# Optimization experiments

Measured on AMD Instinct MI355X. Metric: run time of the kernel, lower is better.

## Reference

```python
import jax, jax.numpy as jnp
import numpy as np
import math

C_S = 384; C_Z = 128; C_H = 16; H = 12; PQ = 4; PV = 8; C_SURF = 16
N_RES = 512; N_SURF = 2048; B = 1
INF = 1e5; EPS = 1e-8
SOFTPLUS_INV_1 = 0.541324854612918


def _quat_to_rot(q):
    q = q / jnp.linalg.norm(q, axis=-1, keepdims=True)
    w, x, y, z = q[..., 0], q[..., 1], q[..., 2], q[..., 3]
    R = jnp.stack([
        1 - 2 * (y * y + z * z), 2 * (x * y - w * z), 2 * (x * z + w * y),
        2 * (x * y + w * z), 1 - 2 * (x * x + z * z), 2 * (y * z - w * x),
        2 * (x * z - w * y), 2 * (y * z + w * x), 1 - 2 * (x * x + y * y),
    ], axis=-1)
    return R.reshape(q.shape[:-1] + (3, 3))


def setup_inputs() -> dict:
    key = jax.random.key(0)
    ks = jax.random.split(key, 32)
    hc = H * C_H            # 192
    hpq = H * PQ * 3        # 144
    hpkv = H * (PQ + PV) * 3  # 432
    cz4 = C_Z // 4
    concat = hc + H * PV * 3 + H * PV + H * cz4 + hc  # 1152
    w = lambda k, i, o: jax.random.normal(k, (i, o), jnp.float32) * 0.02
    inp = {
        's': jax.random.normal(ks[0], (B, N_RES, C_S), jnp.float32),
        'z': jax.random.normal(ks[1], (B, N_RES, N_RES, C_Z), jnp.float32),
        'rots': _quat_to_rot(jax.random.normal(ks[2], (B, N_RES, 4), jnp.float32)),
        'trans': jax.random.normal(ks[3], (B, N_RES, 3), jnp.float32) * 10.0,
        'mask': jnp.ones((B, N_RES), jnp.float32),
        'surface_points': jax.random.normal(ks[4], (B, N_SURF, 3), jnp.float32) * 10.0,
        'surface_features': jax.random.normal(ks[5], (B, N_SURF, C_SURF), jnp.float32),
        'surface_mask': jnp.ones((B, N_SURF), jnp.float32),
        'Wq': w(ks[6], C_S, hc), 'bq': jnp.zeros((hc,)),
        'Wkv': w(ks[7], C_S, 2 * hc), 'bkv': jnp.zeros((2 * hc,)),
        'Wqp': w(ks[8], C_S, hpq), 'bqp': jnp.zeros((hpq,)),
        'Wkvp': w(ks[9], C_S, hpkv), 'bkvp': jnp.zeros((hpkv,)),
        'Wse': w(ks[10], C_SURF, C_S), 'bse': jnp.zeros((C_S,)),
        'Wsq': w(ks[11], C_S, hc), 'bsq': jnp.zeros((hc,)),
        'Wsk': w(ks[12], C_S, hc), 'bsk': jnp.zeros((hc,)),
        'Wsv': w(ks[13], C_S, hc), 'bsv': jnp.zeros((hc,)),
        'Wb': w(ks[14], C_Z, H), 'bb': jnp.zeros((H,)),
        'Wdz': w(ks[15], C_Z, cz4), 'bdz': jnp.zeros((cz4,)),
        'head_weights': jnp.full((H,), SOFTPLUS_INV_1, jnp.float32),
        'sb_weights': jnp.full((1,), SOFTPLUS_INV_1, jnp.float32),
        'Wout': w(ks[16], concat, C_S), 'bout': jnp.zeros((C_S,)),
        'Wso': w(ks[17], 2 * C_S, C_SURF), 'bso': jnp.zeros((C_SURF,)),
    }
    return inp


def reference(s, z, rots, trans, mask, surface_points, surface_features, surface_mask,
              Wq, bq, Wkv, bkv, Wqp, bqp, Wkvp, bkvp, Wse, bse, Wsq, bsq, Wsk, bsk,
              Wsv, bsv, Wb, bb, Wdz, bdz, head_weights, sb_weights, Wout, bout, Wso, bso):
    lin = lambda x, W, b: x @ W + b
    b_, n, _ = s.shape
    m = surface_points.shape[-2]

    surface_feat = lin(surface_features, Wse, bse)                    # [B,M,c_s]
    # backbone<->surface squared distances
    disp = trans[:, :, None, :] - surface_points[:, None, :, :]       # [B,N,M,3]
    dist_sq = jnp.sum(disp * disp, -1)                                # [B,N,M]

    q = lin(s, Wq, bq).reshape(b_, n, H, C_H)
    kv = lin(s, Wkv, bkv).reshape(b_, n, H, 2 * C_H)
    k, v = kv[..., :C_H], kv[..., C_H:]

    # query points: split into 3 coord chunks, stack, rigid-apply
    qp = lin(s, Wqp, bqp)
    qp = jnp.stack(jnp.split(qp, 3, axis=-1), axis=-1)                # [B,N,H*PQ,3]
    qp = jnp.einsum('bnij,bnpj->bnpi', rots, qp) + trans[:, :, None]
    qp = qp.reshape(b_, n, H, PQ, 3)

    kvp = lin(s, Wkvp, bkvp)
    kvp = jnp.stack(jnp.split(kvp, 3, axis=-1), axis=-1)              # [B,N,H*(PQ+PV),3]
    kvp = jnp.einsum('bnij,bnpj->bnpi', rots, kvp) + trans[:, :, None]
    kvp = kvp.reshape(b_, n, H, PQ + PV, 3)
    kp, vp = kvp[..., :PQ, :], kvp[..., PQ:, :]

    b_bias = lin(z, Wb, bb)                                           # [B,N,N,H]
    a = jnp.einsum('bihc,bjhc->bhij', q, k) * math.sqrt(1.0 / (3 * C_H))
    a = a + math.sqrt(1.0 / 3) * jnp.transpose(b_bias, (0, 3, 1, 2))

    # point-distance attention term
    pt = jnp.sum((qp[:, :, None] - kp[:, None]) ** 2, axis=-1)        # [B,N,N,H,PQ]
    hw = jax.nn.softplus(head_weights)                                # [H]
    pt = jnp.sum(pt, axis=-1) * hw * math.sqrt(1.0 / (3 * (PQ * 9.0 / 2))) * (-0.5)
    a = a + jnp.transpose(pt, (0, 3, 1, 2))                           # [B,H,N,N]

    sq_mask = INF * (mask[:, :, None] * mask[:, None, :] - 1.0)
    a = jax.nn.softmax(a + sq_mask[:, None], axis=-1)

    o = jnp.einsum('bhij,bjhc->bihc', a, v).reshape(b_, n, H * C_H)
    o_pt = jnp.einsum('bhij,bjhpd->bihpd', a, vp)                     # [B,N,H,PV,3]
    o_pt = jnp.einsum('bnji,bnhpj->bnhpi', rots, o_pt - trans[:, :, None, None])
    o_pt_norm = jnp.sqrt(jnp.sum(o_pt ** 2, -1) + EPS).reshape(b_, n, H * PV)
    o_pt_flat = o_pt.reshape(b_, n, H * PV, 3)

    pair_z = lin(z, Wdz, bdz)                                         # [B,N,N,cz/4]
    o_pair = jnp.einsum('bhij,bijc->bihc', a, pair_z).reshape(b_, n, -1)

    # surface cross-attention branch
    sq = lin(s, Wsq, bsq).reshape(b_, n, H, C_H)
    sk = lin(surface_feat, Wsk, bsk).reshape(b_, m, H, C_H)
    sv = lin(surface_feat, Wsv, bsv).reshape(b_, m, H, C_H)
    logits = jnp.einsum('bnhc,bmhc->bhnm', sq, sk) * math.sqrt(1.0 / C_H)
    sbw = jax.nn.softplus(sb_weights)[0]
    logits = logits - 0.5 * sbw * dist_sq[:, None]
    cross_mask = mask[:, :, None] * surface_mask[:, None, :]          # [B,N,M]
    logits = logits + INF * (cross_mask - 1.0)[:, None]
    a_s = jax.nn.softmax(logits, axis=-1)
    o_surf = jnp.einsum('bhnm,bmhc->bnhc', a_s, sv).reshape(b_, n, H * C_H)

    o_cat = jnp.concatenate([o, o_pt_flat[..., 0], o_pt_flat[..., 1], o_pt_flat[..., 2],
                             o_pt_norm, o_pair, o_surf], axis=-1)
    s_out = lin(o_cat, Wout, bout)                                    # [B,N,c_s]

    # surface update: attend surface points to backbone (softmax over residues)
    a_ts = jax.nn.softmax(jnp.swapaxes(logits, -1, -2), axis=-1).mean(axis=1)  # [B,M,N]
    s_agg = jnp.einsum('bmn,bnc->bmc', a_ts, s)
    surf_out = lin(jnp.concatenate([surface_feat, s_agg], axis=-1), Wso, bso)
    return s_out, surf_out
```

## Files before the change

### kernel.cpp

```cpp
#include <hip/hip_runtime.h>
#include <cstddef>


#define CS 384
#define INFV 100000.0f

__device__ __forceinline__ float softplusf(float x) { return log1pf(__expf(x)); }

__global__ __launch_bounds__(256) void k_pack(
    const float* __restrict__ Wq, const float* __restrict__ Wsq,
    const float* __restrict__ Wkv, const float* __restrict__ Wqp,
    const float* __restrict__ Wkvp, const float* __restrict__ Wsk,
    const float* __restrict__ Wsv, const float* __restrict__ Wout,
    const float* __restrict__ bq, const float* __restrict__ bsq,
    const float* __restrict__ bkv, const float* __restrict__ bqp,
    const float* __restrict__ bkvp, const float* __restrict__ bsk,
    const float* __restrict__ bsv,
    float* __restrict__ wt1, float* __restrict__ wt2, float* __restrict__ wt3,
    float* __restrict__ b1, float* __restrict__ b2)
{
    const int b = blockIdx.x, t = threadIdx.x;
    if (b >= 1092) {
        int idx = (b - 1092) * 256 + t;
        if (idx < 1344) {
            float v;
            if (idx < 192) v = bq[idx];
            else if (idx < 384) v = bsq[idx - 192];
            else if (idx < 768) v = bkv[idx - 384];
            else if (idx < 912) v = bqp[idx - 768];
            else v = bkvp[idx - 912];
            b1[idx] = v;
        } else if (idx < 1728) {
            int i2 = idx - 1344;
            b2[i2] = (i2 < 192) ? bsk[i2] : bsv[i2 - 192];
        }
        return;
    }
    const float* src; float* dst; int C, coff, tile, ldd;
    if (b < 72)       { src = Wq;   C = 192; dst = wt1; coff = 0;   ldd = 384;  tile = b; }
    else if (b < 144) { src = Wsq;  C = 192; dst = wt1; coff = 192; ldd = 384;  tile = b - 72; }
    else if (b < 288) { src = Wkv;  C = 384; dst = wt1; coff = 384; ldd = 384;  tile = b - 144; }
    else if (b < 348) { src = Wqp;  C = 144; dst = wt1; coff = 768; ldd = 384;  tile = b - 288; }
    else if (b < 516) { src = Wkvp; C = 432; dst = wt1; coff = 912; ldd = 384;  tile = b - 348; }
    else if (b < 588) { src = Wsk;  C = 192; dst = wt2; coff = 0;   ldd = 384;  tile = b - 516; }
    else if (b < 660) { src = Wsv;  C = 192; dst = wt2; coff = 192; ldd = 384;  tile = b - 588; }
    else              { src = Wout; C = 384; dst = wt3; coff = 0;   ldd = 1152; tile = b - 660; }
    const int cT = (C + 31) >> 5;
    const int tk = tile / cT, tc = tile % cT;
    __shared__ float l[32][33];
    const int tr = t >> 5, tcc = t & 31;
    #pragma unroll
    for (int rr = 0; rr < 4; ++rr) {
        int kloc = tr * 4 + rr;
        int cg = tc * 32 + tcc;
        l[kloc][tcc] = (cg < C) ? src[(size_t)(tk * 32 + kloc) * C + cg] : 0.f;
    }
    __syncthreads();
    #pragma unroll
    for (int rr = 0; rr < 4; ++rr) {
        int cloc = tr * 4 + rr;
        int cg = tc * 32 + cloc;
        if (cg < C) dst[(size_t)(coff + cg) * ldd + tk * 32 + tcc] = l[tcc][cloc];
    }
}

__global__ __launch_bounds__(256) void k_transp(
    const float* __restrict__ A, float* __restrict__ At)
{
    __shared__ float tile[32][33];
    const int r0 = blockIdx.y * 32, c0 = blockIdx.x * 32;
    const int tr = threadIdx.x >> 5, tc = threadIdx.x & 31;
    #pragma unroll
    for (int rr = 0; rr < 4; ++rr)
        tile[tr + rr * 8][tc] = A[(size_t)(r0 + tr + rr * 8) * 384 + c0 + tc];
    __syncthreads();
    #pragma unroll
    for (int rr = 0; rr < 4; ++rr)
        At[(size_t)(c0 + tr + rr * 8) * 512 + r0 + tc] = tile[tc][tr + rr * 8];
}

template<int KTOT, bool HB>
__global__ __launch_bounds__(256) void k_gemm(
    const float* __restrict__ A, const float* __restrict__ Wt,
    const float* __restrict__ bias, float* __restrict__ C, int ldc)
{
    __shared__ float As[64][68];
    __shared__ float Ws[64][68];
    const int t = threadIdx.x;
    const int c0 = blockIdx.x * 64, m0 = blockIdx.y * 64;
    const int sr = t >> 4, sk4 = (t & 15) << 2;
    const int wid = t >> 6, lane = t & 63;
    const int wr = (wid >> 1) * 32, wc = (wid & 1) * 32;
    const int lr = lane >> 3, lc = lane & 7;
    float acc[4][4];
    #pragma unroll
    for (int j = 0; j < 4; ++j) {
        float bv = HB ? bias[c0 + wc + lc + 8 * j] : 0.f;
        #pragma unroll
        for (int i = 0; i < 4; ++i) acc[i][j] = bv;
    }
    for (int kc = 0; kc < KTOT; kc += 64) {
        __syncthreads();
        #pragma unroll
        for (int rep = 0; rep < 4; ++rep) {
            int row = sr + rep * 16;
            *(float4*)&As[row][sk4] = *(const float4*)&A[(size_t)(m0 + row) * KTOT + kc + sk4];
            *(float4*)&Ws[row][sk4] = *(const float4*)&Wt[(size_t)(c0 + row) * KTOT + kc + sk4];
        }
        __syncthreads();
        #pragma unroll 4
        for (int k4 = 0; k4 < 16; ++k4) {
            float4 a[4], w[4];
            #pragma unroll
            for (int i = 0; i < 4; ++i) a[i] = *(float4*)&As[wr + lr + 8 * i][k4 * 4];
            #pragma unroll
            for (int j = 0; j < 4; ++j) w[j] = *(float4*)&Ws[wc + lc + 8 * j][k4 * 4];
            #pragma unroll
            for (int i = 0; i < 4; ++i) {
                #pragma unroll
                for (int j = 0; j < 4; ++j) {
                    acc[i][j] = fmaf(a[i].x, w[j].x, acc[i][j]);
                    acc[i][j] = fmaf(a[i].y, w[j].y, acc[i][j]);
                    acc[i][j] = fmaf(a[i].z, w[j].z, acc[i][j]);
                    acc[i][j] = fmaf(a[i].w, w[j].w, acc[i][j]);
                }
            }
        }
    }
    #pragma unroll
    for (int i = 0; i < 4; ++i) {
        #pragma unroll
        for (int j = 0; j < 4; ++j)
            C[(size_t)(m0 + wr + lr + 8 * i) * ldc + c0 + wc + lc + 8 * j] = acc[i][j];
    }
}

__global__ __launch_bounds__(256) void k_scatter(
    const float* __restrict__ proj, const float* __restrict__ rots,
    const float* __restrict__ trans,
    float* __restrict__ qw, float* __restrict__ kw, float* __restrict__ vw,
    float* __restrict__ sqw, float* __restrict__ qpw, float* __restrict__ kpw,
    float* __restrict__ vpw)
{
    __shared__ float p[4][1344];
    const int n0 = blockIdx.x * 4, t = threadIdx.x;
    for (int idx = t; idx < 1344; idx += 256) {
        #pragma unroll
        for (int r = 0; r < 4; ++r) p[r][idx] = proj[(size_t)(n0 + r) * 1344 + idx];
    }
    __syncthreads();
    for (int idx = t; idx < 3072; idx += 256) {
        int r = idx / 768, c = idx % 768;
        int n = n0 + r;
        float v = p[r][c];
        if (c < 192) qw[(size_t)n * 192 + c] = v;
        else if (c < 384) sqw[(size_t)n * 192 + (c - 192)] = v;
        else {
            int cc = c - 384, h = cc >> 5, sub = cc & 31;
            if (sub < 16) kw[(size_t)n * 192 + h * 16 + sub] = v;
            else          vw[(size_t)n * 192 + h * 16 + (sub - 16)] = v;
        }
    }
    for (int idx = t; idx < 2304; idx += 256) {
        int r = idx / 576, rem = idx % 576;
        int n = n0 + r;
        const float* R = &rots[(size_t)n * 9];
        const float* tr = &trans[(size_t)n * 3];
        if (rem < 144) {
            int pp = rem / 3, d = rem % 3;
            float v = fmaf(R[d*3+0], p[r][768 + pp],
                      fmaf(R[d*3+1], p[r][768 + 48 + pp],
                      fmaf(R[d*3+2], p[r][768 + 96 + pp], tr[d])));
            qpw[(size_t)n * 144 + pp * 3 + d] = v;
        } else {
            int rem2 = rem - 144; int pp = rem2 / 3, d = rem2 % 3;
            float v = fmaf(R[d*3+0], p[r][912 + pp],
                      fmaf(R[d*3+1], p[r][912 + 144 + pp],
                      fmaf(R[d*3+2], p[r][912 + 288 + pp], tr[d])));
            int h = pp / 12, ii = pp % 12;
            if (ii < 4) kpw[(size_t)n * 144 + h * 12 + ii * 3 + d] = v;
            else        vpw[(size_t)n * 288 + h * 24 + (ii - 4) * 3 + d] = v;
        }
    }
}

__global__ __launch_bounds__(256) void k_sfeat(
    const float* __restrict__ sf, const float* __restrict__ Wse,
    const float* __restrict__ bse, float* __restrict__ sfeat)
{
    __shared__ float wl[16 * 384];
    __shared__ float sfl[8][16];
    const int m0 = blockIdx.x * 8, t = threadIdx.x;
    for (int idx = t; idx < 6144; idx += 256) wl[idx] = Wse[idx];
    if (t < 128) sfl[t >> 4][t & 15] = sf[(size_t)(m0 + (t >> 4)) * 16 + (t & 15)];
    __syncthreads();
    #pragma unroll
    for (int u = 0; u < 12; ++u) {
        int idx = t + u * 256;
        int r = idx / 384, c = idx % 384;
        float a = bse[c];
        #pragma unroll
        for (int kk = 0; kk < 16; ++kk) a = fmaf(sfl[r][kk], wl[kk * 384 + c], a);
        sfeat[(size_t)(m0 + r) * 384 + c] = a;
    }
}

__global__ __launch_bounds__(256) void k_zpass(
    const float* __restrict__ z, const float* __restrict__ Wb, const float* __restrict__ bb,
    const float* __restrict__ Wdz, const float* __restrict__ bdz, float* __restrict__ bpz)
{
    __shared__ float Wt[44][128];
    __shared__ float bias_s[44];
    __shared__ float zt[64][132];
    const int i = blockIdx.x, t = threadIdx.x;
    const float s3 = 0.5773502691896258f;
    for (int idx = t; idx < 44 * 128; idx += 256) {
        int c = idx >> 7, kk = idx & 127;
        Wt[c][kk] = (c < 12) ? s3 * Wb[kk * 12 + c] : Wdz[kk * 32 + (c - 12)];
    }
    if (t < 44) bias_s[t] = (t < 12) ? s3 * bb[t] : bdz[t - 12];
    const int jl = t & 63, cg = t >> 6;
    for (int j0 = 0; j0 < 512; j0 += 64) {
        __syncthreads();
        for (int idx = t; idx < 2048; idx += 256) {
            int r = idx >> 5, c4 = (idx & 31) << 2;
            *(float4*)&zt[r][c4] = *(const float4*)&z[((size_t)i * 512 + j0 + r) * 128 + c4];
        }
        __syncthreads();
        float acc[11];
        #pragma unroll
        for (int u = 0; u < 11; ++u) acc[u] = bias_s[cg * 11 + u];
        #pragma unroll 2
        for (int k4 = 0; k4 < 128; k4 += 4) {
            float4 zv = *(float4*)&zt[jl][k4];
            #pragma unroll
            for (int u = 0; u < 11; ++u) {
                float4 wv = *(float4*)&Wt[cg * 11 + u][k4];
                acc[u] = fmaf(zv.x, wv.x, acc[u]);
                acc[u] = fmaf(zv.y, wv.y, acc[u]);
                acc[u] = fmaf(zv.z, wv.z, acc[u]);
                acc[u] = fmaf(zv.w, wv.w, acc[u]);
            }
        }
        #pragma unroll
        for (int u = 0; u < 11; ++u)
            bpz[((size_t)i * 44 + cg * 11 + u) * 512 + j0 + jl] = acc[u];
    }
}

__global__ __launch_bounds__(256) void k_attn(
    const float* __restrict__ qw, const float* __restrict__ kw, const float* __restrict__ vw,
    const float* __restrict__ qpw, const float* __restrict__ kpw, const float* __restrict__ vpw,
    const float* __restrict__ bpz, const float* __restrict__ mask,
    const float* __restrict__ rots, const float* __restrict__ trans,
    const float* __restrict__ hwp, float* __restrict__ ocat)
{
    __shared__ float pls[12 * 516];
    __shared__ float qs[192], qps[144], opt[288], cpt[12], red[4];
    const int i = blockIdx.x, t = threadIdx.x;
    if (t < 192) qs[t] = qw[(size_t)i * 192 + t];
    if (t < 144) qps[t] = qpw[(size_t)i * 144 + t];
    if (t < 12) cpt[t] = -0.5f * 0.13608276348795434f * softplusf(hwp[t]);
    const float mask_i = mask[i];
    __syncthreads();
    for (int hj = t; hj < 6144; hj += 256) {
        int h = hj >> 9, j = hj & 511;
        float kj[16], kpj[12];
        { const float4* kr = (const float4*)&kw[(size_t)j * 192 + h * 16];
          *(float4*)&kj[0] = kr[0]; *(float4*)&kj[4] = kr[1];
          *(float4*)&kj[8] = kr[2]; *(float4*)&kj[12] = kr[3]; }
        { const float4* kr = (const float4*)&kpw[(size_t)j * 144 + h * 12];
          *(float4*)&kpj[0] = kr[0]; *(float4*)&kpj[4] = kr[1]; *(float4*)&kpj[8] = kr[2]; }
        float qk = 0.f;
        #pragma unroll
        for (int c = 0; c < 16; ++c) qk = fmaf(qs[h * 16 + c], kj[c], qk);
        float pts = 0.f;
        #pragma unroll
        for (int p = 0; p < 4; ++p) {
            float dx = qps[h*12+p*3+0] - kpj[p*3+0];
            float dy = qps[h*12+p*3+1] - kpj[p*3+1];
            float dz = qps[h*12+p*3+2] - kpj[p*3+2];
            pts += dx*dx + dy*dy + dz*dz;
        }
        float lg = fmaf(0.14433756729740643f, qk, bpz[((size_t)i * 44 + h) * 512 + j]);
        lg = fmaf(cpt[h], pts, lg);
        lg += INFV * (mask_i * mask[j] - 1.0f);
        pls[h * 516 + j] = lg;
    }
    __syncthreads();
    for (int h = 0; h < 12; ++h) {
        float v0 = pls[h * 516 + t], v1 = pls[h * 516 + 256 + t];
        float mx = fmaxf(v0, v1);
        #pragma unroll
        for (int off = 32; off; off >>= 1) mx = fmaxf(mx, __shfl_xor(mx, off));
        if ((t & 63) == 0) red[t >> 6] = mx;
        __syncthreads();
        mx = fmaxf(fmaxf(red[0], red[1]), fmaxf(red[2], red[3]));
        __syncthreads();
        float e0 = __expf(v0 - mx), e1 = __expf(v1 - mx);
        float sm = e0 + e1;
        #pragma unroll
        for (int off = 32; off; off >>= 1) sm += __shfl_xor(sm, off);
        if ((t & 63) == 0) red[t >> 6] = sm;
        __syncthreads();
        float inv = 1.0f / (red[0] + red[1] + red[2] + red[3]);
        pls[h * 516 + t] = e0 * inv;
        pls[h * 516 + 256 + t] = e1 * inv;
        __syncthreads();
    }
    for (int rnd = 0; rnd < 2; ++rnd) {
        int oi = t + rnd * 256;
        if (oi < 480) {
            int h, stride; const float* src;
            if (oi < 192) { h = oi >> 4; src = vw + oi; stride = 192; }
            else { h = (oi - 192) / 24; src = vpw + (oi - 192); stride = 288; }
            const float* pr = &pls[h * 516];
            float a0 = 0, a1 = 0, a2 = 0, a3 = 0;
            for (int j = 0; j < 512; j += 4) {
                a0 = fmaf(pr[j+0], src[(size_t)(j+0) * stride], a0);
                a1 = fmaf(pr[j+1], src[(size_t)(j+1) * stride], a1);
                a2 = fmaf(pr[j+2], src[(size_t)(j+2) * stride], a2);
                a3 = fmaf(pr[j+3], src[(size_t)(j+3) * stride], a3);
            }
            float acc = (a0 + a1) + (a2 + a3);
            if (oi < 192) ocat[(size_t)i * 1152 + oi] = acc;
            else opt[oi - 192] = acc;
        }
    }
    {
        int w = t >> 6, lane = t & 63;
        for (int u = 0; u < 96; ++u) {
            int oi = w * 96 + u; int h = oi >> 5, c = oi & 31;
            const float* pz = &bpz[((size_t)i * 44 + 12 + c) * 512];
            const float* pr = &pls[h * 516];
            float sacc = 0.f;
            #pragma unroll
            for (int jj = 0; jj < 8; ++jj)
                sacc = fmaf(pr[lane + jj * 64], pz[lane + jj * 64], sacc);
            #pragma unroll
            for (int off = 32; off; off >>= 1) sacc += __shfl_xor(sacc, off);
            if (lane == 0) ocat[(size_t)i * 1152 + 576 + oi] = sacc;
        }
    }
    __syncthreads();
    if (t < 96) {
        int h = t >> 3, p = t & 7;
        const float* R = &rots[(size_t)i * 9];
        float gx = opt[h*24 + p*3 + 0] - trans[(size_t)i*3 + 0];
        float gy = opt[h*24 + p*3 + 1] - trans[(size_t)i*3 + 1];
        float gz = opt[h*24 + p*3 + 2] - trans[(size_t)i*3 + 2];
        float lx = R[0]*gx + R[3]*gy + R[6]*gz;
        float ly = R[1]*gx + R[4]*gy + R[7]*gz;
        float lz = R[2]*gx + R[5]*gy + R[8]*gz;
        float nm = sqrtf(lx*lx + ly*ly + lz*lz + 1e-8f);
        int col = h * 8 + p;
        size_t base = (size_t)i * 1152;
        ocat[base + 192 + col] = lx;
        ocat[base + 288 + col] = ly;
        ocat[base + 384 + col] = lz;
        ocat[base + 480 + col] = nm;
    }
}

__global__ __launch_bounds__(256) void k_surf(
    const float* __restrict__ sqw, const float* __restrict__ skv,
    const float* __restrict__ trans, const float* __restrict__ mask,
    const float* __restrict__ sp, const float* __restrict__ smask,
    const float* __restrict__ sbwp, float* __restrict__ ocat)
{
    __shared__ float sk_t[256][17];
    __shared__ float sv_t[256][17];
    __shared__ float sp_t[768];
    __shared__ float smask_t[256];
    const int h = blockIdx.x >> 5;
    const int n0 = (blockIdx.x & 31) * 16;
    const int t = threadIdx.x;
    const int tn = t >> 4, tm = t & 15;
    const int n = n0 + tn;
    const float sbw = softplusf(sbwp[0]);
    float qreg[16];
    #pragma unroll
    for (int c = 0; c < 16; ++c) qreg[c] = sqw[(size_t)n * 192 + h * 16 + c];
    const float trx = trans[(size_t)n*3+0], tryy = trans[(size_t)n*3+1], trz = trans[(size_t)n*3+2];
    const float mask_n = mask[n];
    float mx = -1e30f, l = 0.f;
    float acc[16];
    #pragma unroll
    for (int c = 0; c < 16; ++c) acc[c] = 0.f;
    for (int tile = 0; tile < 8; ++tile) {
        __syncthreads();
        const int mb = tile * 256;
        for (int idx = t; idx < 1024; idx += 256) {
            int ml = idx >> 2, c4 = (idx & 3) << 2;
            float4 v4 = *(const float4*)&skv[(size_t)(mb + ml) * 384 + h * 16 + c4];
            sk_t[ml][c4+0]=v4.x; sk_t[ml][c4+1]=v4.y; sk_t[ml][c4+2]=v4.z; sk_t[ml][c4+3]=v4.w;
            float4 w4 = *(const float4*)&skv[(size_t)(mb + ml) * 384 + 192 + h * 16 + c4];
            sv_t[ml][c4+0]=w4.x; sv_t[ml][c4+1]=w4.y; sv_t[ml][c4+2]=w4.z; sv_t[ml][c4+3]=w4.w;
        }
        for (int idx = t; idx < 768; idx += 256) sp_t[idx] = sp[(size_t)mb * 3 + idx];
        smask_t[t] = smask[mb + t];
        __syncthreads();
        float lgr[16];
        float tmax = -1e30f;
        #pragma unroll
        for (int kk = 0; kk < 16; ++kk) {
            int ml = tm + (kk << 4);
            float dot = 0.f;
            #pragma unroll
            for (int c = 0; c < 16; ++c) dot = fmaf(qreg[c], sk_t[ml][c], dot);
            float dx = trx - sp_t[ml*3+0], dy = tryy - sp_t[ml*3+1], dz = trz - sp_t[ml*3+2];
            float lg = fmaf(0.25f, dot, -0.5f * sbw * (dx*dx + dy*dy + dz*dz));
            lg += INFV * (mask_n * smask_t[ml] - 1.0f);
            lgr[kk] = lg;
            tmax = fmaxf(tmax, lg);
        }
        float mn = fmaxf(mx, tmax);
        float scale = __expf(mx - mn);
        l *= scale;
        #pragma unroll
        for (int c = 0; c < 16; ++c) acc[c] *= scale;
        #pragma unroll
        for (int kk = 0; kk < 16; ++kk) {
            int ml = tm + (kk << 4);
            float w = __expf(lgr[kk] - mn);
            l += w;
            #pragma unroll
            for (int c = 0; c < 16; ++c) acc[c] = fmaf(w, sv_t[ml][c], acc[c]);
        }
        mx = mn;
    }
    #pragma unroll
    for (int off = 1; off < 16; off <<= 1) {
        float m2 = __shfl_xor(mx, off), l2 = __shfl_xor(l, off);
        float mn = fmaxf(mx, m2);
        float e1 = __expf(mx - mn), e2 = __expf(m2 - mn);
        l = l * e1 + l2 * e2;
        #pragma unroll
        for (int c = 0; c < 16; ++c) {
            float a2 = __shfl_xor(acc[c], off);
            acc[c] = acc[c] * e1 + a2 * e2;
        }
        mx = mn;
    }
    const float invl = 1.0f / l;
    float outv = 0.f;
    #pragma unroll
    for (int c = 0; c < 16; ++c) if (tm == c) outv = acc[c];
    ocat[(size_t)n * 1152 + 960 + h * 16 + tm] = outv * invl;
}

__global__ __launch_bounds__(256) void k_tlog(
    const float* __restrict__ sqw, const float* __restrict__ skv,
    const float* __restrict__ trans, const float* __restrict__ mask,
    const float* __restrict__ sp, const float* __restrict__ smask,
    const float* __restrict__ sbwp, float* __restrict__ logits,
    float* __restrict__ stat_m, float* __restrict__ stat_il)
{
    __shared__ float sk_s[32][16];
    __shared__ float sq_s[32][16];
    __shared__ float trans_s[96];
    __shared__ float mask_s[32];
    __shared__ float spm_s[96];
    __shared__ float smask_s[32];
    const int h = blockIdx.y;
    const int m0 = blockIdx.x * 32;
    const int t = threadIdx.x;
    const int tmg = t >> 5, tnl = t & 31;
    const float sbw = softplusf(sbwp[0]);
    for (int idx = t; idx < 512; idx += 256) {
        int row = idx >> 4, c = idx & 15;
        sk_s[row][c] = skv[(size_t)(m0 + row) * 384 + h * 16 + c];
    }
    if (t < 96) spm_s[t] = sp[(size_t)m0 * 3 + t];
    if (t < 32) smask_s[t] = smask[m0 + t];
    __syncthreads();
    float skr[4][16];
    float spx[4], spy[4], spz[4], smk[4];
    #pragma unroll
    for (int mi = 0; mi < 4; ++mi) {
        int row = tmg * 4 + mi;
        #pragma unroll
        for (int c4 = 0; c4 < 16; c4 += 4)
            *(float4*)&skr[mi][c4] = *(float4*)&sk_s[row][c4];
        spx[mi] = spm_s[row*3+0]; spy[mi] = spm_s[row*3+1]; spz[mi] = spm_s[row*3+2];
        smk[mi] = smask_s[row];
    }
    float mxr[4], lr[4];
    #pragma unroll
    for (int mi = 0; mi < 4; ++mi) { mxr[mi] = -1e30f; lr[mi] = 0.f; }
    for (int nt = 0; nt < 16; ++nt) {
        __syncthreads();
        const int nb = nt * 32;
        if (t < 128) {
            int nn = t >> 2, c4 = (t & 3) << 2;
            *(float4*)&sq_s[nn][c4] = *(const float4*)&sqw[(size_t)(nb + nn) * 192 + h * 16 + c4];
        }
        if (t < 96) trans_s[t] = trans[(size_t)nb * 3 + t];
        if (t < 32) mask_s[t] = mask[nb + t];
        __syncthreads();
        float q[16];
        #pragma unroll
        for (int c4 = 0; c4 < 16; c4 += 4)
            *(float4*)&q[c4] = *(float4*)&sq_s[tnl][c4];
        const float tx = trans_s[tnl*3+0], ty = trans_s[tnl*3+1], tz = trans_s[tnl*3+2];
        const float mkn = mask_s[tnl];
        #pragma unroll
        for (int mi = 0; mi < 4; ++mi) {
            float dot = 0.f;
            #pragma unroll
            for (int c = 0; c < 16; ++c) dot = fmaf(skr[mi][c], q[c], dot);
            float dx = tx - spx[mi], dy = ty - spy[mi], dz = tz - spz[mi];
            float mterm = INFV * (mkn * smk[mi] - 1.0f) - 0.5f * sbw * (dx*dx + dy*dy + dz*dz);
            float lg = fmaf(0.25f, dot, mterm);
            logits[((size_t)(m0 + tmg * 4 + mi) * 12 + h) * 512 + nb + tnl] = lg;
            float newm = fmaxf(mxr[mi], lg);
            lr[mi] = lr[mi] * __expf(mxr[mi] - newm) + __expf(lg - newm);
            mxr[mi] = newm;
        }
    }
    #pragma unroll
    for (int off = 1; off < 32; off <<= 1) {
        #pragma unroll
        for (int mi = 0; mi < 4; ++mi) {
            float m2 = __shfl_xor(mxr[mi], off), l2 = __shfl_xor(lr[mi], off);
            float newm = fmaxf(mxr[mi], m2);
            lr[mi] = lr[mi] * __expf(mxr[mi] - newm) + l2 * __expf(m2 - newm);
            mxr[mi] = newm;
        }
    }
    if (tnl == 0) {
        #pragma unroll
        for (int mi = 0; mi < 4; ++mi) {
            int m = m0 + tmg * 4 + mi;
            stat_m[(size_t)m * 12 + h] = mxr[mi];
            stat_il[(size_t)m * 12 + h] = 1.0f / lr[mi];
        }
    }
}

__global__ __launch_bounds__(256) void k_tw(
    const float* __restrict__ logits, const float* __restrict__ stat_m,
    const float* __restrict__ stat_il, float* __restrict__ w)
{
    __shared__ float mxs[12], ils[12];
    const int m = blockIdx.x, t = threadIdx.x;
    if (t < 12) { mxs[t] = stat_m[(size_t)m * 12 + t]; ils[t] = stat_il[(size_t)m * 12 + t]; }
    __syncthreads();
    const float* lp = logits + (size_t)m * 12 * 512;
    float a0 = 0.f, a1 = 0.f;
    #pragma unroll
    for (int h = 0; h < 12; ++h) {
        a0 += __expf(lp[h * 512 + t] - mxs[h]) * ils[h];
        a1 += __expf(lp[h * 512 + 256 + t] - mxs[h]) * ils[h];
    }
    w[(size_t)m * 512 + t] = a0 * (1.0f / 12.0f);
    w[(size_t)m * 512 + 256 + t] = a1 * (1.0f / 12.0f);
}

__global__ __launch_bounds__(256) void k_surf_out(
    const float* __restrict__ sfeat, const float* __restrict__ saggw,
    const float* __restrict__ Wso, const float* __restrict__ bso,
    float* __restrict__ out)
{
    __shared__ float wl[12304];
    const int t = threadIdx.x;
    for (int idx = t; idx < 12288; idx += 256) {
        int k = idx >> 4, c = idx & 15;
        wl[(k / 192) * 3076 + (k % 192) * 16 + c] = Wso[idx];
    }
    const int m = blockIdx.x * 64 + (t >> 2);
    const int kq = t & 3;
    const float* src = (kq < 2) ? &sfeat[(size_t)m * 384 + kq * 192]
                                : &saggw[(size_t)m * 384 + (kq - 2) * 192];
    __syncthreads();
    float acc[16];
    #pragma unroll
    for (int c = 0; c < 16; ++c) acc[c] = 0.f;
    const float* wb = &wl[kq * 3076];
    for (int k = 0; k < 192; k += 4) {
        float4 v = *(const float4*)&src[k];
        #pragma unroll
        for (int e = 0; e < 4; ++e) {
            float sv = (&v.x)[e];
            #pragma unroll
            for (int c = 0; c < 16; ++c)
                acc[c] = fmaf(sv, wb[(k + e) * 16 + c], acc[c]);
        }
    }
    #pragma unroll
    for (int c = 0; c < 16; ++c) {
        acc[c] += __shfl_xor(acc[c], 1);
        acc[c] += __shfl_xor(acc[c], 2);
    }
    #pragma unroll
    for (int c = 0; c < 16; ++c) {
        if ((c >> 2) == kq) out[196608 + (size_t)m * 16 + c] = acc[c] + bso[c];
    }
}

extern "C" void kernel_launch(void* const* d_in, const int* in_sizes, int n_in,
                              void* d_out, int out_size, void* d_ws, size_t ws_size,
                              hipStream_t stream)
{
    (void)in_sizes; (void)n_in; (void)out_size; (void)ws_size;
    const float* s     = (const float*)d_in[0];
    const float* z     = (const float*)d_in[1];
    const float* rots  = (const float*)d_in[2];
    const float* trans = (const float*)d_in[3];
    const float* mask  = (const float*)d_in[4];
    const float* sp    = (const float*)d_in[5];
    const float* sf    = (const float*)d_in[6];
    const float* smask = (const float*)d_in[7];
    const float* Wq    = (const float*)d_in[8];  const float* bq   = (const float*)d_in[9];
    const float* Wkv   = (const float*)d_in[10]; const float* bkv  = (const float*)d_in[11];
    const float* Wqp   = (const float*)d_in[12]; const float* bqp  = (const float*)d_in[13];
    const float* Wkvp  = (const float*)d_in[14]; const float* bkvp = (const float*)d_in[15];
    const float* Wse   = (const float*)d_in[16]; const float* bse  = (const float*)d_in[17];
    const float* Wsq   = (const float*)d_in[18]; const float* bsq  = (const float*)d_in[19];
    const float* Wsk   = (const float*)d_in[20]; const float* bsk  = (const float*)d_in[21];
    const float* Wsv   = (const float*)d_in[22]; const float* bsv  = (const float*)d_in[23];
    const float* Wb    = (const float*)d_in[24]; const float* bb   = (const float*)d_in[25];
    const float* Wdz   = (const float*)d_in[26]; const float* bdz  = (const float*)d_in[27];
    const float* hw    = (const float*)d_in[28]; const float* sbw  = (const float*)d_in[29];
    const float* Wout  = (const float*)d_in[30]; const float* bout = (const float*)d_in[31];
    const float* Wso   = (const float*)d_in[32]; const float* bso  = (const float*)d_in[33];
    float* out = (float*)d_out;

    float* qw    = (float*)d_ws;
    float* kw    = qw    + (size_t)512 * 192;
    float* vw    = kw    + (size_t)512 * 192;
    float* sqw   = vw    + (size_t)512 * 192;
    float* qpw   = sqw   + (size_t)512 * 192;
    float* kpw   = qpw   + (size_t)512 * 144;
    float* vpw   = kpw   + (size_t)512 * 144;
    float* sfeat = vpw   + (size_t)512 * 288;
    float* skv   = sfeat + (size_t)2048 * 384;
    float* ocat  = skv   + (size_t)2048 * 384;
    float* sagg  = ocat  + (size_t)512 * 1152;
    float* region = sagg + (size_t)2048 * 384;
    float* proj   = region;
    float* bpz    = region;
    float* logits = region;
    float* wt1   = region + (size_t)2048 * 12 * 512;
    float* wt2   = wt1   + (size_t)1344 * 384;
    float* wt3   = wt2   + (size_t)384 * 384;
    float* b1    = wt3   + (size_t)384 * 1152;
    float* b2    = b1    + 1344;
    float* st    = b2    + 384;
    float* wbuf  = st    + (size_t)384 * 512;
    float* statm = wbuf  + (size_t)2048 * 512;
    float* stati = statm + (size_t)2048 * 12;

    k_pack<<<dim3(1099), dim3(256), 0, stream>>>(Wq, Wsq, Wkv, Wqp, Wkvp, Wsk, Wsv, Wout,
        bq, bsq, bkv, bqp, bkvp, bsk, bsv, wt1, wt2, wt3, b1, b2);
    k_transp<<<dim3(12, 16), dim3(256), 0, stream>>>(s, st);
    k_gemm<384, true><<<dim3(21, 8), dim3(256), 0, stream>>>(s, wt1, b1, proj, 1344);
    k_scatter<<<dim3(128), dim3(256), 0, stream>>>(proj, rots, trans,
        qw, kw, vw, sqw, qpw, kpw, vpw);
    k_sfeat<<<dim3(256), dim3(256), 0, stream>>>(sf, Wse, bse, sfeat);
    k_gemm<384, true><<<dim3(6, 32), dim3(256), 0, stream>>>(sfeat, wt2, b2, skv, 384);
    k_zpass<<<dim3(512), dim3(256), 0, stream>>>(z, Wb, bb, Wdz, bdz, bpz);
    k_attn<<<dim3(512), dim3(256), 0, stream>>>(qw, kw, vw, qpw, kpw, vpw, bpz, mask,
        rots, trans, hw, ocat);
    k_surf<<<dim3(384), dim3(256), 0, stream>>>(sqw, skv, trans, mask, sp, smask,
        sbw, ocat);
    k_tlog<<<dim3(64, 12), dim3(256), 0, stream>>>(sqw, skv, trans, mask, sp, smask,
        sbw, logits, statm, stati);
    k_tw<<<dim3(2048), dim3(256), 0, stream>>>(logits, statm, stati, wbuf);
    k_gemm<512, false><<<dim3(6, 32), dim3(256), 0, stream>>>(wbuf, st, nullptr, sagg, 384);
    k_surf_out<<<dim3(32), dim3(256), 0, stream>>>(sfeat, sagg, Wso, bso, out);
    k_gemm<1152, true><<<dim3(6, 8), dim3(256), 0, stream>>>(ocat, wt3, bout, out, 384);
}
```

Baseline: 524.3 us.

## Split IPA attention into logits/softmax, pair, value-GEMM and finalize kernels

The monolithic per-residue attention kernel is split into four stages. Logits and softmax run per (residue, head-group) and write probabilities to a global buffer. A separate pair-aggregation kernel reads those probabilities, and a tiled GEMM computes the scalar and point value outputs with V rows reused across 64 query rows. A small finalize kernel scatters the results and applies the inverse frame transform. The aim is to replace the uncoalesced strided V reads and serial per-head softmax barriers with better parallelism and reuse. The cost is a 12x512x512 probability buffer written and re-read twice, plus extra launches.

```diff
diff --git a/kernel.cpp b/kernel.cpp
--- a/kernel.cpp
+++ b/kernel.cpp
@@ -248,23 +248,26 @@
     }
 }
 
-__global__ __launch_bounds__(256) void k_attn(
-    const float* __restrict__ qw, const float* __restrict__ kw, const float* __restrict__ vw,
-    const float* __restrict__ qpw, const float* __restrict__ kpw, const float* __restrict__ vpw,
+__global__ __launch_bounds__(256) void k_attn_a(
+    const float* __restrict__ qw, const float* __restrict__ kw,
+    const float* __restrict__ qpw, const float* __restrict__ kpw,
     const float* __restrict__ bpz, const float* __restrict__ mask,
-    const float* __restrict__ rots, const float* __restrict__ trans,
-    const float* __restrict__ hwp, float* __restrict__ ocat)
-{
-    __shared__ float pls[12 * 516];
-    __shared__ float qs[192], qps[144], opt[288], cpt[12], red[4];
-    const int i = blockIdx.x, t = threadIdx.x;
-    if (t < 192) qs[t] = qw[(size_t)i * 192 + t];
-    if (t < 144) qps[t] = qpw[(size_t)i * 144 + t];
-    if (t < 12) cpt[t] = -0.5f * 0.13608276348795434f * softplusf(hwp[t]);
+    const float* __restrict__ hwp, float* __restrict__ abuf)
+{
+    __shared__ float pls[4][520];
+    __shared__ float qs[64], qps[48], cpt4[4];
+    const int i = blockIdx.x, hg = blockIdx.y;
+    const int t = threadIdx.x;
+    if (t < 64) qs[t] = qw[(size_t)i * 192 + hg * 64 + t];
+    if (t < 48) qps[t] = qpw[(size_t)i * 144 + hg * 48 + t];
+    if (t < 4) cpt4[t] = -0.5f * 0.13608276348795434f * softplusf(hwp[hg * 4 + t]);
     const float mask_i = mask[i];
     __syncthreads();
-    for (int hj = t; hj < 6144; hj += 256) {
-        int h = hj >> 9, j = hj & 511;
+    #pragma unroll 2
+    for (int it = 0; it < 8; ++it) {
+        int idx = t + it * 256;
+        int hh = idx >> 9, j = idx & 511;
+        int h = hg * 4 + hh;
         float kj[16], kpj[12];
         { const float4* kr = (const float4*)&kw[(size_t)j * 192 + h * 16];
           *(float4*)&kj[0] = kr[0]; *(float4*)&kj[4] = kr[1];
@@ -273,82 +276,149 @@
           *(float4*)&kpj[0] = kr[0]; *(float4*)&kpj[4] = kr[1]; *(float4*)&kpj[8] = kr[2]; }
         float qk = 0.f;
         #pragma unroll
-        for (int c = 0; c < 16; ++c) qk = fmaf(qs[h * 16 + c], kj[c], qk);
+        for (int c = 0; c < 16; ++c) qk = fmaf(qs[hh * 16 + c], kj[c], qk);
         float pts = 0.f;
         #pragma unroll
         for (int p = 0; p < 4; ++p) {
-            float dx = qps[h*12+p*3+0] - kpj[p*3+0];
-            float dy = qps[h*12+p*3+1] - kpj[p*3+1];
-            float dz = qps[h*12+p*3+2] - kpj[p*3+2];
+            float dx = qps[hh*12+p*3+0] - kpj[p*3+0];
+            float dy = qps[hh*12+p*3+1] - kpj[p*3+1];
+            float dz = qps[hh*12+p*3+2] - kpj[p*3+2];
             pts += dx*dx + dy*dy + dz*dz;
         }
         float lg = fmaf(0.14433756729740643f, qk, bpz[((size_t)i * 44 + h) * 512 + j]);
-        lg = fmaf(cpt[h], pts, lg);
+        lg = fmaf(cpt4[hh], pts, lg);
         lg += INFV * (mask_i * mask[j] - 1.0f);
-        pls[h * 516 + j] = lg;
-    }
-    __syncthreads();
-    for (int h = 0; h < 12; ++h) {
-        float v0 = pls[h * 516 + t], v1 = pls[h * 516 + 256 + t];
-        float mx = fmaxf(v0, v1);
-        #pragma unroll
-        for (int off = 32; off; off >>= 1) mx = fmaxf(mx, __shfl_xor(mx, off));
-        if ((t & 63) == 0) red[t >> 6] = mx;
-        __syncthreads();
-        mx = fmaxf(fmaxf(red[0], red[1]), fmaxf(red[2], red[3]));
-        __syncthreads();
-        float e0 = __expf(v0 - mx), e1 = __expf(v1 - mx);
-        float sm = e0 + e1;
-        #pragma unroll
-        for (int off = 32; off; off >>= 1) sm += __shfl_xor(sm, off);
-        if ((t & 63) == 0) red[t >> 6] = sm;
-        __syncthreads();
-        float inv = 1.0f / (red[0] + red[1] + red[2] + red[3]);
-        pls[h * 516 + t] = e0 * inv;
-        pls[h * 516 + 256 + t] = e1 * inv;
-        __syncthreads();
-    }
-    for (int rnd = 0; rnd < 2; ++rnd) {
-        int oi = t + rnd * 256;
-        if (oi < 480) {
-            int h, stride; const float* src;
-            if (oi < 192) { h = oi >> 4; src = vw + oi; stride = 192; }
-            else { h = (oi - 192) / 24; src = vpw + (oi - 192); stride = 288; }
-            const float* pr = &pls[h * 516];
-            float a0 = 0, a1 = 0, a2 = 0, a3 = 0;
-            for (int j = 0; j < 512; j += 4) {
-                a0 = fmaf(pr[j+0], src[(size_t)(j+0) * stride], a0);
-                a1 = fmaf(pr[j+1], src[(size_t)(j+1) * stride], a1);
-                a2 = fmaf(pr[j+2], src[(size_t)(j+2) * stride], a2);
-                a3 = fmaf(pr[j+3], src[(size_t)(j+3) * stride], a3);
+        pls[hh][j] = lg;
+    }
+    __syncthreads();
+    const int w = t >> 6, lane = t & 63;
+    float v[8];
+    #pragma unroll
+    for (int k = 0; k < 8; ++k) v[k] = pls[w][lane + k * 64];
+    float mx = v[0];
+    #pragma unroll
+    for (int k = 1; k < 8; ++k) mx = fmaxf(mx, v[k]);
+    #pragma unroll
+    for (int off = 32; off; off >>= 1) mx = fmaxf(mx, __shfl_xor(mx, off));
+    float sm = 0.f;
+    #pragma unroll
+    for (int k = 0; k < 8; ++k) { v[k] = __expf(v[k] - mx); sm += v[k]; }
+    #pragma unroll
+    for (int off = 32; off; off >>= 1) sm += __shfl_xor(sm, off);
+    const float inv = 1.0f / sm;
+    float* dst = abuf + ((size_t)(hg * 4 + w) * 512 + i) * 512;
+    #pragma unroll
+    for (int k = 0; k < 8; ++k) dst[lane + k * 64] = v[k] * inv;
+}
+
+__global__ __launch_bounds__(256) void k_attn_pair(
+    const float* __restrict__ abuf, const float* __restrict__ bpz,
+    float* __restrict__ ocat)
+{
+    __shared__ float al[12][512];
+    const int i = blockIdx.x, t = threadIdx.x;
+    #pragma unroll
+    for (int u = 0; u < 12; ++u) {
+        al[u][t] = abuf[(size_t)u * 262144 + (size_t)i * 512 + t];
+        al[u][t + 256] = abuf[(size_t)u * 262144 + (size_t)i * 512 + t + 256];
+    }
+    __syncthreads();
+    const int c = t & 31;
+    const int h1 = t >> 5;
+    const bool dual = (t < 128);
+    const float* pz = bpz + ((size_t)i * 44 + 12 + c) * 512;
+    const float* a1 = al[h1];
+    const float* a2 = al[dual ? h1 + 8 : 0];
+    float acc1 = 0.f, acc2 = 0.f;
+    for (int j = 0; j < 512; j += 4) {
+        float4 p = *(const float4*)&pz[j];
+        acc1 = fmaf(a1[j+0], p.x, acc1);
+        acc1 = fmaf(a1[j+1], p.y, acc1);
+        acc1 = fmaf(a1[j+2], p.z, acc1);
+        acc1 = fmaf(a1[j+3], p.w, acc1);
+        if (dual) {
+            acc2 = fmaf(a2[j+0], p.x, acc2);
+            acc2 = fmaf(a2[j+1], p.y, acc2);
+            acc2 = fmaf(a2[j+2], p.z, acc2);
+            acc2 = fmaf(a2[j+3], p.w, acc2);
+        }
+    }
+    ocat[(size_t)i * 1152 + 576 + h1 * 32 + c] = acc1;
+    if (dual) ocat[(size_t)i * 1152 + 576 + (h1 + 8) * 32 + c] = acc2;
+}
+
+__global__ __launch_bounds__(256) void k_gemm_ov(
+    const float* __restrict__ abuf, const float* __restrict__ vw,
+    const float* __restrict__ vpw, float* __restrict__ cbuf)
+{
+    __shared__ float As[64][68];
+    __shared__ float Bs[64][44];
+    const int i0 = blockIdx.x * 64, h = blockIdx.y;
+    const int t = threadIdx.x;
+    const int sr = t >> 4, sk4 = (t & 15) << 2;
+    const int r1 = t >> 3;
+    const int cb = t & 7;
+    float acc[2][5];
+    #pragma unroll
+    for (int u = 0; u < 5; ++u) { acc[0][u] = 0.f; acc[1][u] = 0.f; }
+    for (int kc = 0; kc < 512; kc += 64) {
+        __syncthreads();
+        #pragma unroll
+        for (int rep = 0; rep < 4; ++rep) {
+            int row = sr + rep * 16;
+            *(float4*)&As[row][sk4] =
+                *(const float4*)&abuf[(size_t)h * 262144 + (size_t)(i0 + row) * 512 + kc + sk4];
+        }
+        #pragma unroll
+        for (int u = 0; u < 10; ++u) {
+            int idx = t + u * 256;
+            int r = idx / 40, cc = idx % 40;
+            Bs[r][cc] = (cc < 16) ? vw[(size_t)(kc + r) * 192 + h * 16 + cc]
+                                  : vpw[(size_t)(kc + r) * 288 + h * 24 + (cc - 16)];
+        }
+        __syncthreads();
+        #pragma unroll 4
+        for (int kk = 0; kk < 64; ++kk) {
+            float av1 = As[r1][kk], av2 = As[r1 + 32][kk];
+            #pragma unroll
+            for (int u = 0; u < 5; ++u) {
+                float b = Bs[kk][cb + 8 * u];
+                acc[0][u] = fmaf(av1, b, acc[0][u]);
+                acc[1][u] = fmaf(av2, b, acc[1][u]);
             }
-            float acc = (a0 + a1) + (a2 + a3);
-            if (oi < 192) ocat[(size_t)i * 1152 + oi] = acc;
-            else opt[oi - 192] = acc;
-        }
-    }
-    {
-        int w = t >> 6, lane = t & 63;
-        for (int u = 0; u < 96; ++u) {
-            int oi = w * 96 + u; int h = oi >> 5, c = oi & 31;
-            const float* pz = &bpz[((size_t)i * 44 + 12 + c) * 512];
-            const float* pr = &pls[h * 516];
-            float sacc = 0.f;
-            #pragma unroll
-            for (int jj = 0; jj < 8; ++jj)
-                sacc = fmaf(pr[lane + jj * 64], pz[lane + jj * 64], sacc);
-            #pragma unroll
-            for (int off = 32; off; off >>= 1) sacc += __shfl_xor(sacc, off);
-            if (lane == 0) ocat[(size_t)i * 1152 + 576 + oi] = sacc;
-        }
-    }
-    __syncthreads();
-    if (t < 96) {
-        int h = t >> 3, p = t & 7;
+        }
+    }
+    #pragma unroll
+    for (int u = 0; u < 5; ++u) {
+        cbuf[((size_t)h * 512 + i0 + r1) * 40 + cb + 8 * u] = acc[0][u];
+        cbuf[((size_t)h * 512 + i0 + r1 + 32) * 40 + cb + 8 * u] = acc[1][u];
+    }
+}
+
+__global__ __launch_bounds__(256) void k_optfin(
+    const float* __restrict__ cbuf, const float* __restrict__ rots,
+    const float* __restrict__ trans, float* __restrict__ ocat)
+{
+    __shared__ float cl[4][12][40];
+    const int i0 = blockIdx.x * 4, t = threadIdx.x;
+    for (int idx = t; idx < 1920; idx += 256) {
+        int ii = idx / 480, rem = idx % 480;
+        int h = rem / 40, c = rem % 40;
+        cl[ii][h][c] = cbuf[((size_t)h * 512 + i0 + ii) * 40 + c];
+    }
+    __syncthreads();
+    for (int idx = t; idx < 768; idx += 256) {
+        int ii = idx / 192, o = idx % 192;
+        ocat[(size_t)(i0 + ii) * 1152 + o] = cl[ii][o >> 4][o & 15];
+    }
+    for (int idx = t; idx < 384; idx += 256) {
+        int ii = idx / 96, hp = idx % 96;
+        int h = hp >> 3, p = hp & 7;
+        int i = i0 + ii;
         const float* R = &rots[(size_t)i * 9];
-        float gx = opt[h*24 + p*3 + 0] - trans[(size_t)i*3 + 0];
-        float gy = opt[h*24 + p*3 + 1] - trans[(size_t)i*3 + 1];
-        float gz = opt[h*24 + p*3 + 2] - trans[(size_t)i*3 + 2];
+        float gx = cl[ii][h][16 + p*3 + 0] - trans[(size_t)i*3 + 0];
+        float gy = cl[ii][h][16 + p*3 + 1] - trans[(size_t)i*3 + 1];
+        float gz = cl[ii][h][16 + p*3 + 2] - trans[(size_t)i*3 + 2];
         float lx = R[0]*gx + R[3]*gy + R[6]*gz;
         float ly = R[1]*gx + R[4]*gy + R[7]*gz;
         float lz = R[2]*gx + R[5]*gy + R[8]*gz;
@@ -650,6 +720,8 @@
     float* wbuf  = st    + (size_t)384 * 512;
     float* statm = wbuf  + (size_t)2048 * 512;
     float* stati = statm + (size_t)2048 * 12;
+    float* abuf  = stati + (size_t)2048 * 12;
+    float* cbuf  = abuf  + (size_t)12 * 512 * 512;
 
     k_pack<<<dim3(1099), dim3(256), 0, stream>>>(Wq, Wsq, Wkv, Wqp, Wkvp, Wsk, Wsv, Wout,
         bq, bsq, bkv, bqp, bkvp, bsk, bsv, wt1, wt2, wt3, b1, b2);
@@ -660,8 +732,10 @@
     k_sfeat<<<dim3(256), dim3(256), 0, stream>>>(sf, Wse, bse, sfeat);
     k_gemm<384, true><<<dim3(6, 32), dim3(256), 0, stream>>>(sfeat, wt2, b2, skv, 384);
     k_zpass<<<dim3(512), dim3(256), 0, stream>>>(z, Wb, bb, Wdz, bdz, bpz);
-    k_attn<<<dim3(512), dim3(256), 0, stream>>>(qw, kw, vw, qpw, kpw, vpw, bpz, mask,
-        rots, trans, hw, ocat);
+    k_attn_a<<<dim3(512, 3), dim3(256), 0, stream>>>(qw, kw, qpw, kpw, bpz, mask, hw, abuf);
+    k_attn_pair<<<dim3(512), dim3(256), 0, stream>>>(abuf, bpz, ocat);
+    k_gemm_ov<<<dim3(8, 12), dim3(256), 0, stream>>>(abuf, vw, vpw, cbuf);
+    k_optfin<<<dim3(128), dim3(256), 0, stream>>>(cbuf, rots, trans, ocat);
     k_surf<<<dim3(384), dim3(256), 0, stream>>>(sqw, skv, trans, mask, sp, smask,
         sbw, ocat);
     k_tlog<<<dim3(64, 12), dim3(256), 0, stream>>>(sqw, skv, trans, mask, sp, smask,
```

After: 571.3 us, median of 4. +9.0%, slower.
